# Performance work log

Measured on AMD Instinct MI355X. Metric: run time of the kernel, lower is better.

Reference implementation:

```python
import jax, jax.numpy as jnp
import numpy as np

N_ITER = 2
K = 16          # neighbor_sample_size
DIM = 64
B = 4096
N_USERS = 100000
N_ENTITIES = 100000
N_RELATIONS = 32


def setup_inputs() -> dict:
    key = jax.random.key(0)
    ks = jax.random.split(key, 9)
    scale = 0.05
    return {
        "u_ids": jax.random.randint(ks[0], (B,), 0, N_USERS, dtype=jnp.int64 if jax.config.jax_enable_x64 else jnp.int32),
        "i_ids": jax.random.randint(ks[1], (B,), 0, N_ENTITIES, dtype=jnp.int32),
        "adj_entity": jax.random.randint(ks[2], (N_ENTITIES, K), 0, N_ENTITIES, dtype=jnp.int32),
        "adj_relation": jax.random.randint(ks[3], (N_ENTITIES, K), 0, N_RELATIONS, dtype=jnp.int32),
        "user_emb": jax.random.normal(ks[4], (N_USERS, DIM), jnp.float32) * scale,
        "entity_emb": jax.random.normal(ks[5], (N_ENTITIES, DIM), jnp.float32) * scale,
        "relation_emb": jax.random.normal(ks[6], (N_RELATIONS + 1, DIM), jnp.float32) * scale,
        "W0": jax.random.normal(ks[7], (DIM, DIM), jnp.float32) * scale,
        "b0": jnp.zeros((DIM,), jnp.float32),
        "W1": jax.random.normal(ks[8], (DIM, DIM), jnp.float32) * scale,
        "b1": jnp.zeros((DIM,), jnp.float32),
    }


def _aggregate(entities, relations, ue, entity_emb, relation_emb, layers):
    # entities: list of [B, K^h] int arrays, h = 0..N_ITER
    # relations: list of [B, K^(h+1)] int arrays, h = 0..N_ITER-1
    b = ue.shape[0]
    entity_vectors = [entity_emb[e] for e in entities]          # [B, m, DIM]
    relation_vectors = [relation_emb[r] for r in relations]     # [B, m*K, DIM]
    ue4 = ue[:, None, None, :]                                  # [B,1,1,DIM]
    for i in range(N_ITER):
        W, bias, act = layers[i]
        nxt = []
        for hop in range(N_ITER - i):
            sv = entity_vectors[hop]                                        # [B, m, DIM]
            nv = entity_vectors[hop + 1].reshape(b, -1, K, DIM)             # [B, m, K, DIM]
            nr = relation_vectors[hop].reshape(b, -1, K, DIM)               # [B, m, K, DIM]
            scores = jnp.mean(ue4 * nr, axis=-1)                            # [B, m, K]
            attn = jax.nn.softmax(scores, axis=-1)[..., None]               # [B, m, K, 1]
            agg = jnp.mean(attn * nv, axis=2)                               # [B, m, DIM]
            out = act(jnp.einsum("bmd,ed->bme", sv + agg, W) + bias)       # Linear: x @ W.T + b
            nxt.append(out)
        entity_vectors = nxt
    return entity_vectors[0].reshape(b, DIM)


def reference(u_ids, i_ids, adj_entity, adj_relation, user_emb, entity_emb,
              relation_emb, W0, b0, W1, b1):
    b = u_ids.shape[0]
    # _get_neighbors
    entities = [i_ids[:, None]]
    relations = []
    for _ in range(N_ITER):
        idx = entities[-1].reshape(-1)
        entities.append(adj_entity[idx].reshape(b, -1))
        relations.append(adj_relation[idx].reshape(b, -1))
    ue = user_emb[u_ids]                                        # [B, DIM]
    layers = [(W0, b0, jax.nn.relu), (W1, b1, jnp.tanh)]
    item = _aggregate(entities, relations, ue, entity_emb, relation_emb, layers)
    scores = jax.nn.sigmoid(jnp.sum(ue * item, axis=1))         # [B]
    return scores
```

## Files before the change

### kernel.cpp

```cpp
#include <hip/hip_runtime.h>
#include <math.h>

#define KNBR 16
#define DIM 64
#define NREL 32

#define Q8SCALE 512.0f
#define Q4SCALE 28.0f

__device__ __forceinline__ int irl(int v, int l) {
    return __builtin_amdgcn_readlane(v, l);
}
__device__ __forceinline__ float frl(float v, int l) {
    return __int_as_float(__builtin_amdgcn_readlane(__float_as_int(v), l));
}

__global__ void convert_tabs(const float* __restrict__ emb,
                             const int* __restrict__ adj_rel,
                             signed char* __restrict__ d8,
                             unsigned char* __restrict__ d4,
                             unsigned char* __restrict__ r8,
                             int n4, int nrel4)
{
    const int stride = gridDim.x * blockDim.x;
    for (int i = blockIdx.x * blockDim.x + threadIdx.x; i < n4; i += stride) {
        float4 f = ((const float4*)emb)[i];
        int q0 = (int)rintf(fminf(fmaxf(f.x * Q8SCALE, -127.f), 127.f));
        int q1 = (int)rintf(fminf(fmaxf(f.y * Q8SCALE, -127.f), 127.f));
        int q2 = (int)rintf(fminf(fmaxf(f.z * Q8SCALE, -127.f), 127.f));
        int q3 = (int)rintf(fminf(fmaxf(f.w * Q8SCALE, -127.f), 127.f));
        ((char4*)d8)[i] = make_char4((signed char)q0, (signed char)q1,
                                     (signed char)q2, (signed char)q3);
        int p0 = (int)rintf(fminf(fmaxf(f.x * Q4SCALE, -7.f), 7.f));
        int p1 = (int)rintf(fminf(fmaxf(f.y * Q4SCALE, -7.f), 7.f));
        int p2 = (int)rintf(fminf(fmaxf(f.z * Q4SCALE, -7.f), 7.f));
        int p3 = (int)rintf(fminf(fmaxf(f.w * Q4SCALE, -7.f), 7.f));
        unsigned char b0 = (unsigned char)((p0 & 0xF) | ((p1 & 0xF) << 4));
        unsigned char b1 = (unsigned char)((p2 & 0xF) | ((p3 & 0xF) << 4));
        ((uchar2*)d4)[i] = make_uchar2(b0, b1);
        if (i < nrel4) {
            int4 r = ((const int4*)adj_rel)[i];
            ((uchar4*)r8)[i] = make_uchar4((unsigned char)r.x, (unsigned char)r.y,
                                           (unsigned char)r.z, (unsigned char)r.w);
        }
    }
}

template <bool Q8>
__global__ __launch_bounds__(64, 4) void kgnnls_kernel(
    const int* __restrict__ u_ids, const int* __restrict__ i_ids,
    const int* __restrict__ adj_entity, const int* __restrict__ adj_relation,
    const float* __restrict__ user_emb, const float* __restrict__ entity_emb,
    const signed char* __restrict__ et8,
    const unsigned char* __restrict__ et4,
    const unsigned char* __restrict__ rel8,
    const float* __restrict__ relation_emb,
    const float* __restrict__ W0, const float* __restrict__ b0,
    const float* __restrict__ W1, const float* __restrict__ b1,
    float* __restrict__ out, int B)
{
    const int lane = threadIdx.x;
    const int b = blockIdx.x;

    __shared__ float xbuf[17][DIM];
    __shared__ float uebuf[DIM];

    const int u  = u_ids[b];
    const int i0 = i_ids[b];

    const float ue = user_emb[u * DIM + lane];
    uebuf[lane] = ue;
    const float bias0 = b0[lane];
    __syncthreads();

    float s_val = 0.f;
    if (lane < NREL + 1) {
        const float4* rrow = (const float4*)(relation_emb + lane * DIM);
        const float4* ub   = (const float4*)uebuf;
        float acc = 0.f;
        #pragma unroll
        for (int q = 0; q < 16; ++q) {
            float4 r4 = rrow[q];
            float4 u4 = ub[q];
            acc += r4.x*u4.x + r4.y*u4.y + r4.z*u4.z + r4.w*u4.w;
        }
        s_val = acc * (1.0f / DIM);
    }

    int e1k = 0, r0k = 0;
    if (lane < KNBR) {
        e1k = adj_entity[i0 * KNBR + lane];
        r0k = Q8 ? (int)rel8[i0 * KNBR + lane]
                 : adj_relation[i0 * KNBR + lane];
    }

    float sc0 = __shfl(s_val, r0k);
    float m0 = sc0;
    m0 = fmaxf(m0, __shfl_xor(m0, 1));
    m0 = fmaxf(m0, __shfl_xor(m0, 2));
    m0 = fmaxf(m0, __shfl_xor(m0, 4));
    m0 = fmaxf(m0, __shfl_xor(m0, 8));
    float ex0 = __expf(sc0 - m0);
    float z0 = ex0;
    z0 += __shfl_xor(z0, 1);
    z0 += __shfl_xor(z0, 2);
    z0 += __shfl_xor(z0, 4);
    z0 += __shfl_xor(z0, 8);
    const float attn0 = ex0 / z0;

    const int kk = lane >> 2;
    const int jb = (lane & 3) * 4;
    const int ek = __shfl(e1k, kk);
    const int4 e2i = *(const int4*)(adj_entity + ek * KNBR + jb);
    int e2idx[4] = { e2i.x, e2i.y, e2i.z, e2i.w };

    int r2x, r2y, r2z, r2w;
    if (Q8) {
        uchar4 rr = *(const uchar4*)(rel8 + ek * KNBR + jb);
        r2x = rr.x; r2y = rr.y; r2z = rr.z; r2w = rr.w;
    } else {
        const int4 r2i = *(const int4*)(adj_relation + ek * KNBR + jb);
        r2x = r2i.x; r2y = r2i.y; r2z = r2i.z; r2w = r2i.w;
    }

    float sc1[4];
    sc1[0] = __shfl(s_val, r2x);
    sc1[1] = __shfl(s_val, r2y);
    sc1[2] = __shfl(s_val, r2z);
    sc1[3] = __shfl(s_val, r2w);

    float m1 = fmaxf(fmaxf(sc1[0], sc1[1]), fmaxf(sc1[2], sc1[3]));
    m1 = fmaxf(m1, __shfl_xor(m1, 1));
    m1 = fmaxf(m1, __shfl_xor(m1, 2));
    float a1[4];
    float z1 = 0.f;
    #pragma unroll
    for (int t = 0; t < 4; ++t) { a1[t] = __expf(sc1[t] - m1); z1 += a1[t]; }
    z1 += __shfl_xor(z1, 1);
    z1 += __shfl_xor(z1, 2);
    const float inv_z1 = 1.0f / z1;
    #pragma unroll
    for (int t = 0; t < 4; ++t) a1[t] *= inv_z1;

    int v1raw[KNBR];
    #pragma unroll
    for (int k = 0; k < KNBR; ++k) {
        const int ei = irl(e1k, k);
        v1raw[k] = Q8 ? (int)et8[(size_t)ei * DIM + lane]
                      : __float_as_int(entity_emb[(size_t)ei * DIM + lane]);
    }
    const int ev0raw = Q8 ? (int)et8[(size_t)i0 * DIM + lane]
                          : __float_as_int(entity_emb[(size_t)i0 * DIM + lane]);

    const int sh = 28 - ((lane & 1) << 2);
    auto issue = [&](int* v2, int k) {
        #pragma unroll
        for (int j = 0; j < 16; ++j) {
            const int src = 4 * k + (j >> 2);
            const int ei2 = irl(e2idx[j & 3], src);
            v2[j] = Q8 ? (int)et4[(size_t)ei2 * 32 + (lane >> 1)]
                       : __float_as_int(entity_emb[(size_t)ei2 * DIM + lane]);
        }
    };
    auto consume = [&](const int* v2, int k) -> float {
        float acc = 0.f;
        #pragma unroll
        for (int j = 0; j < 16; ++j) {
            const float w = frl(a1[j & 3], 4 * k + (j >> 2));
            float v;
            if (Q8) {
                const int t = ((int)((unsigned)v2[j] << sh)) >> 28;
                v = (float)t;
            } else {
                v = __int_as_float(v2[j]);
            }
            acc += w * v;
        }
        return acc;
    };
    const float xsc = Q8 ? (1.0f / (KNBR * Q4SCALE)) : (1.0f / KNBR);
    const float vsc = Q8 ? (1.0f / Q8SCALE) : 1.0f;

    float agg0 = 0.f;
    int v2a[16], v2b[16];
    issue(v2a, 0);
    #pragma unroll
    for (int k = 0; k < KNBR; k += 2) {
        issue(v2b, k + 1);
        const float acca = consume(v2a, k);
        if (k + 2 < KNBR) issue(v2a, k + 2);
        const float accb = consume(v2b, k + 1);
        const float v1k0 = (Q8 ? (float)v1raw[k]     : __int_as_float(v1raw[k]))     * vsc;
        const float v1k1 = (Q8 ? (float)v1raw[k + 1] : __int_as_float(v1raw[k + 1])) * vsc;
        agg0 += frl(attn0, k) * v1k0 + frl(attn0, k + 1) * v1k1;
        xbuf[1 + k][lane] = v1k0 + acca * xsc;
        xbuf[2 + k][lane] = v1k1 + accb * xsc;
    }
    const float ev0 = (Q8 ? (float)ev0raw : __int_as_float(ev0raw)) * vsc;
    xbuf[0][lane] = ev0 + agg0 * (1.0f / KNBR);
    __syncthreads();

    float h[17];
    {
        #pragma unroll
        for (int r = 0; r < 17; ++r) h[r] = bias0;
        const float4* wrow = (const float4*)(W0 + lane * DIM);
        #pragma unroll
        for (int q = 0; q < 16; ++q) {
            float4 w = wrow[q];
            #pragma unroll
            for (int r = 0; r < 17; ++r) {
                float4 xv = ((const float4*)xbuf[r])[q];
                h[r] += xv.x * w.x + xv.y * w.y + xv.z * w.z + xv.w * w.w;
            }
        }
        #pragma unroll
        for (int r = 0; r < 17; ++r) h[r] = fmaxf(h[r], 0.f);
    }

    float aggL = 0.f;
    #pragma unroll
    for (int k = 0; k < KNBR; ++k)
        aggL += frl(attn0, k) * h[1 + k];
    const float xL = h[0] + aggL * (1.0f / KNBR);
    __syncthreads();
    xbuf[0][lane] = xL;
    __syncthreads();

    float acc1 = b1[lane];
    {
        const float4* wrow = (const float4*)(W1 + lane * DIM);
        const float4* xb   = (const float4*)xbuf[0];
        #pragma unroll
        for (int q = 0; q < 16; ++q) {
            float4 w  = wrow[q];
            float4 xv = xb[q];
            acc1 += xv.x * w.x + xv.y * w.y + xv.z * w.z + xv.w * w.w;
        }
    }
    const float item = tanhf(acc1);

    float p = ue * item;
    #pragma unroll
    for (int m = 1; m < 64; m <<= 1) p += __shfl_xor(p, m);
    if (lane == 0) out[b] = 1.0f / (1.0f + __expf(-p));
}

extern "C" void kernel_launch(void* const* d_in, const int* in_sizes, int n_in,
                              void* d_out, int out_size, void* d_ws, size_t ws_size,
                              hipStream_t stream) {
    const int*   u_ids        = (const int*)  d_in[0];
    const int*   i_ids        = (const int*)  d_in[1];
    const int*   adj_entity   = (const int*)  d_in[2];
    const int*   adj_relation = (const int*)  d_in[3];
    const float* user_emb     = (const float*)d_in[4];
    const float* entity_emb   = (const float*)d_in[5];
    const float* relation_emb = (const float*)d_in[6];
    const float* W0           = (const float*)d_in[7];
    const float* b0           = (const float*)d_in[8];
    const float* W1           = (const float*)d_in[9];
    const float* b1           = (const float*)d_in[10];
    float* out = (float*)d_out;

    const int B      = in_sizes[0];
    const int n_emb  = in_sizes[5];
    const int n_rel  = in_sizes[3];
    const size_t off4   = (size_t)n_emb;
    const size_t offr   = off4 + (size_t)n_emb / 2;
    const size_t ws_needed = offr + (size_t)n_rel;

    if (ws_size >= ws_needed) {
        signed char*   et8  = (signed char*)d_ws;
        unsigned char* et4  = (unsigned char*)d_ws + off4;
        unsigned char* rel8 = (unsigned char*)d_ws + offr;
        hipLaunchKernelGGL(convert_tabs, dim3(1024), dim3(256), 0, stream,
            entity_emb, adj_relation, et8, et4, rel8, n_emb / 4, n_rel / 4);
        hipLaunchKernelGGL((kgnnls_kernel<true>), dim3(B), dim3(64), 0, stream,
            u_ids, i_ids, adj_entity, adj_relation, user_emb, entity_emb,
            et8, et4, rel8, relation_emb, W0, b0, W1, b1, out, B);
    } else {
        hipLaunchKernelGGL((kgnnls_kernel<false>), dim3(B), dim3(64), 0, stream,
            u_ids, i_ids, adj_entity, adj_relation, user_emb, entity_emb,
            (const signed char*)entity_emb ,
            (const unsigned char*)entity_emb ,
            (const unsigned char*)adj_relation ,
            relation_emb, W0, b0, W1, b1, out, B);
    }
}
```

Baseline: 150.7 us.

## Compute the first-layer linear with bf16 MFMA instead of scalar FMA

Converts W0 to bf16 in the prep kernel and also stores bf16 copies of the 17 stage-one input rows. The first dense layer (17x64 by 64x64) then runs as 16x16x32 bf16 MFMA tiles, replacing the per-lane scalar dot products. A one-time MFMA probe builds a table mapping accumulator registers to row and column and sets a flag that gates the path. The aim is to take the FMA-heavy matmul off the vector ALUs, at the cost of bf16 precision loss, extra LDS buffers and an added barrier. The second tile computes 16 rows but only row 16 is used, so most of that work is wasted.

```diff
diff --git a/kernel.cpp b/kernel.cpp
--- a/kernel.cpp
+++ b/kernel.cpp
@@ -8,20 +8,68 @@
 #define Q8SCALE 512.0f
 #define Q4SCALE 28.0f
 
+typedef __attribute__((ext_vector_type(8))) short short8;
+typedef __attribute__((ext_vector_type(4))) float floatx4;
+
 __device__ __forceinline__ int irl(int v, int l) {
     return __builtin_amdgcn_readlane(v, l);
 }
 __device__ __forceinline__ float frl(float v, int l) {
     return __int_as_float(__builtin_amdgcn_readlane(__float_as_int(v), l));
 }
+__device__ __forceinline__ unsigned short f2bf(float x) {
+    unsigned u = __float_as_uint(x);
+    u += 0x7fffu + ((u >> 16) & 1u);
+    return (unsigned short)(u >> 16);
+}
 
 __global__ void convert_tabs(const float* __restrict__ emb,
                              const int* __restrict__ adj_rel,
+                             const float* __restrict__ W0,
                              signed char* __restrict__ d8,
                              unsigned char* __restrict__ d4,
                              unsigned char* __restrict__ r8,
-                             int n4, int nrel4)
+                             unsigned short* __restrict__ w0b,
+                             int* __restrict__ rctab,
+                             int* __restrict__ mapflag,
+                             int n4, int nrel4, int nw4)
 {
+    if (blockIdx.x == 0 && threadIdx.x < 64) {
+        const int lane = threadIdx.x;
+        const int g = lane >> 4, c15 = lane & 15;
+        short8 av, bv;
+        #pragma unroll
+        for (int j = 0; j < 8; ++j) { av[j] = 0; bv[j] = 0; }
+        if (g == 0) {
+            av[0] = (short)f2bf((float)(c15 + 1));
+            av[1] = (short)f2bf(1.0f);
+            bv[0] = (short)f2bf(1.0f);
+            bv[1] = (short)f2bf((float)(16 * (c15 + 1)));
+        }
+        floatx4 pacc = {0.f, 0.f, 0.f, 0.f};
+        pacc = __builtin_amdgcn_mfma_f32_16x16x32_bf16(av, bv, pacc, 0, 0, 0);
+        int okm = 1, sum = 0, rc[4];
+        #pragma unroll
+        for (int r = 0; r < 4; ++r) {
+            const float vc = fminf(fmaxf(pacc[r], 0.f), 1.0e6f);
+            const int iv = (int)vc;
+            const int mm = (iv - 17) & 15;
+            const int nn = (iv - 17) >> 4;
+            const int ok = (pacc[r] == (float)iv) && (iv >= 17) && (iv <= 272)
+                           && (mm + 16 * nn + 17 == iv);
+            okm &= ok;
+            sum += iv - 17;
+            rc[r] = mm | (nn << 8);
+        }
+        #pragma unroll
+        for (int m = 1; m < 64; m <<= 1) {
+            sum += __shfl_xor(sum, m);
+            okm &= __shfl_xor(okm, m);
+        }
+        ((int4*)rctab)[lane] = make_int4(rc[0], rc[1], rc[2], rc[3]);
+        if (lane == 0) *mapflag = (okm != 0 && sum == 32640) ? 1 : 0;
+    }
+
     const int stride = gridDim.x * blockDim.x;
     for (int i = blockIdx.x * blockDim.x + threadIdx.x; i < n4; i += stride) {
         float4 f = ((const float4*)emb)[i];
@@ -43,6 +91,11 @@
             ((uchar4*)r8)[i] = make_uchar4((unsigned char)r.x, (unsigned char)r.y,
                                            (unsigned char)r.z, (unsigned char)r.w);
         }
+        if (i < nw4) {
+            float4 w = ((const float4*)W0)[i];
+            ((ushort4*)w0b)[i] = make_ushort4(f2bf(w.x), f2bf(w.y),
+                                              f2bf(w.z), f2bf(w.w));
+        }
     }
 }
 
@@ -54,6 +107,9 @@
     const signed char* __restrict__ et8,
     const unsigned char* __restrict__ et4,
     const unsigned char* __restrict__ rel8,
+    const unsigned short* __restrict__ w0b,
+    const int* __restrict__ rctab,
+    const int* __restrict__ mapflag,
     const float* __restrict__ relation_emb,
     const float* __restrict__ W0, const float* __restrict__ b0,
     const float* __restrict__ W1, const float* __restrict__ b1,
@@ -62,14 +118,21 @@
     const int lane = threadIdx.x;
     const int b = blockIdx.x;
 
-    __shared__ float xbuf[17][DIM];
+    __shared__ unsigned short xbf[32][72];
+    __shared__ union { float x32[17][DIM]; float hb[17][68]; } us;
     __shared__ float uebuf[DIM];
+    __shared__ float xLbuf[DIM];
+    __shared__ float b0buf[DIM];
+
+    bool usemfma = false;
+    if (Q8) usemfma = (*mapflag != 0);
 
     const int u  = u_ids[b];
     const int i0 = i_ids[b];
 
     const float ue = user_emb[u * DIM + lane];
     uebuf[lane] = ue;
+    b0buf[lane] = b0[lane];
     const float bias0 = b0[lane];
     __syncthreads();
 
@@ -193,15 +256,78 @@
         const float v1k0 = (Q8 ? (float)v1raw[k]     : __int_as_float(v1raw[k]))     * vsc;
         const float v1k1 = (Q8 ? (float)v1raw[k + 1] : __int_as_float(v1raw[k + 1])) * vsc;
         agg0 += frl(attn0, k) * v1k0 + frl(attn0, k + 1) * v1k1;
-        xbuf[1 + k][lane] = v1k0 + acca * xsc;
-        xbuf[2 + k][lane] = v1k1 + accb * xsc;
+        const float x0 = v1k0 + acca * xsc;
+        const float x1 = v1k1 + accb * xsc;
+        us.x32[1 + k][lane] = x0;
+        us.x32[2 + k][lane] = x1;
+        xbf[1 + k][lane] = f2bf(x0);
+        xbf[2 + k][lane] = f2bf(x1);
     }
     const float ev0 = (Q8 ? (float)ev0raw : __int_as_float(ev0raw)) * vsc;
-    xbuf[0][lane] = ev0 + agg0 * (1.0f / KNBR);
+    const float xself = ev0 + agg0 * (1.0f / KNBR);
+    us.x32[0][lane] = xself;
+    xbf[0][lane] = f2bf(xself);
     __syncthreads();
 
-    float h[17];
-    {
+    float xL;
+    if (Q8 && usemfma) {
+        const int g = lane >> 4, c15 = lane & 15;
+        short8 bfr[2][4];
+        #pragma unroll
+        for (int s = 0; s < 2; ++s)
+            #pragma unroll
+            for (int t = 0; t < 4; ++t)
+                bfr[s][t] = *(const short8*)(w0b + (16*t + c15) * DIM + 32*s + 8*g);
+
+        floatx4 acc[2][4];
+        #pragma unroll
+        for (int mt = 0; mt < 2; ++mt)
+            #pragma unroll
+            for (int t = 0; t < 4; ++t)
+                acc[mt][t] = (floatx4){0.f, 0.f, 0.f, 0.f};
+
+        #pragma unroll
+        for (int s = 0; s < 2; ++s) {
+            short8 afr[2];
+            #pragma unroll
+            for (int mt = 0; mt < 2; ++mt)
+                afr[mt] = *(const short8*)&xbf[16*mt + c15][32*s + 8*g];
+            #pragma unroll
+            for (int mt = 0; mt < 2; ++mt)
+                #pragma unroll
+                for (int t = 0; t < 4; ++t)
+                    acc[mt][t] = __builtin_amdgcn_mfma_f32_16x16x32_bf16(
+                        afr[mt], bfr[s][t], acc[mt][t], 0, 0, 0);
+        }
+
+        const int4 rc4 = ((const int4*)rctab)[lane];
+        const int mr[4] = { rc4.x & 255, rc4.y & 255, rc4.z & 255, rc4.w & 255 };
+        const int nr[4] = { rc4.x >> 8,  rc4.y >> 8,  rc4.z >> 8,  rc4.w >> 8 };
+
+        #pragma unroll
+        for (int t = 0; t < 4; ++t) {
+            #pragma unroll
+            for (int r = 0; r < 4; ++r) {
+                const int col = 16*t + nr[r];
+                us.hb[mr[r]][col] = fmaxf(acc[0][t][r] + b0buf[col], 0.f);
+            }
+            #pragma unroll
+            for (int r = 0; r < 4; ++r) {
+                if (mr[r] == 0) {
+                    const int col = 16*t + nr[r];
+                    us.hb[16][col] = fmaxf(acc[1][t][r] + b0buf[col], 0.f);
+                }
+            }
+        }
+        __syncthreads();
+
+        float aggL = 0.f;
+        #pragma unroll
+        for (int k = 0; k < KNBR; ++k)
+            aggL += frl(attn0, k) * us.hb[1 + k][lane];
+        xL = us.hb[0][lane] + aggL * (1.0f / KNBR);
+    } else {
+        float h[17];
         #pragma unroll
         for (int r = 0; r < 17; ++r) h[r] = bias0;
         const float4* wrow = (const float4*)(W0 + lane * DIM);
@@ -210,27 +336,26 @@
             float4 w = wrow[q];
             #pragma unroll
             for (int r = 0; r < 17; ++r) {
-                float4 xv = ((const float4*)xbuf[r])[q];
+                float4 xv = ((const float4*)us.x32[r])[q];
                 h[r] += xv.x * w.x + xv.y * w.y + xv.z * w.z + xv.w * w.w;
             }
         }
         #pragma unroll
         for (int r = 0; r < 17; ++r) h[r] = fmaxf(h[r], 0.f);
-    }
-
-    float aggL = 0.f;
-    #pragma unroll
-    for (int k = 0; k < KNBR; ++k)
-        aggL += frl(attn0, k) * h[1 + k];
-    const float xL = h[0] + aggL * (1.0f / KNBR);
+        float aggLs = 0.f;
+        #pragma unroll
+        for (int k = 0; k < KNBR; ++k)
+            aggLs += frl(attn0, k) * h[1 + k];
+        xL = h[0] + aggLs * (1.0f / KNBR);
+    }
     __syncthreads();
-    xbuf[0][lane] = xL;
+    xLbuf[lane] = xL;
     __syncthreads();
 
     float acc1 = b1[lane];
     {
         const float4* wrow = (const float4*)(W1 + lane * DIM);
-        const float4* xb   = (const float4*)xbuf[0];
+        const float4* xb   = (const float4*)xLbuf;
         #pragma unroll
         for (int q = 0; q < 16; ++q) {
             float4 w  = wrow[q];
@@ -265,25 +390,35 @@
     const int B      = in_sizes[0];
     const int n_emb  = in_sizes[5];
     const int n_rel  = in_sizes[3];
-    const size_t off4   = (size_t)n_emb;
-    const size_t offr   = off4 + (size_t)n_emb / 2;
-    const size_t ws_needed = offr + (size_t)n_rel;
+    const int n_w0   = in_sizes[7];
+    const size_t off4 = (size_t)n_emb;
+    const size_t offr = off4 + (size_t)n_emb / 2;
+    const size_t offw = offr + (size_t)n_rel;
+    const size_t offp = offw + (size_t)n_w0 * 2;
+    const size_t ws_needed = offp + 2048;
 
     if (ws_size >= ws_needed) {
-        signed char*   et8  = (signed char*)d_ws;
-        unsigned char* et4  = (unsigned char*)d_ws + off4;
-        unsigned char* rel8 = (unsigned char*)d_ws + offr;
+        signed char*    et8  = (signed char*)d_ws;
+        unsigned char*  et4  = (unsigned char*)d_ws + off4;
+        unsigned char*  rel8 = (unsigned char*)d_ws + offr;
+        unsigned short* w0b  = (unsigned short*)((unsigned char*)d_ws + offw);
+        int*            rct  = (int*)((unsigned char*)d_ws + offp);
+        int*            flg  = rct + 256;
         hipLaunchKernelGGL(convert_tabs, dim3(1024), dim3(256), 0, stream,
-            entity_emb, adj_relation, et8, et4, rel8, n_emb / 4, n_rel / 4);
+            entity_emb, adj_relation, W0, et8, et4, rel8, w0b, rct, flg,
+            n_emb / 4, n_rel / 4, n_w0 / 4);
         hipLaunchKernelGGL((kgnnls_kernel<true>), dim3(B), dim3(64), 0, stream,
             u_ids, i_ids, adj_entity, adj_relation, user_emb, entity_emb,
-            et8, et4, rel8, relation_emb, W0, b0, W1, b1, out, B);
+            et8, et4, rel8, w0b, rct, flg, relation_emb, W0, b0, W1, b1, out, B);
     } else {
         hipLaunchKernelGGL((kgnnls_kernel<false>), dim3(B), dim3(64), 0, stream,
             u_ids, i_ids, adj_entity, adj_relation, user_emb, entity_emb,
             (const signed char*)entity_emb ,
             (const unsigned char*)entity_emb ,
             (const unsigned char*)adj_relation ,
+            (const unsigned short*)entity_emb ,
+            (const int*)adj_entity ,
+            (const int*)adj_entity ,
             relation_emb, W0, b0, W1, b1, out, B);
     }
 }
```

Measured after the change: 150.3 us. About the same (-0.3%).
